# Kernel optimization log

Measured on AMD Instinct MI355X. Metric: run time of the kernel, lower is better.

The kernel has to match this reference:

```python
import jax, jax.numpy as jnp
import numpy as np

D_MODEL = 1024
HEAD_SIZE = 64
BLOCK_SIZE = 2048
B, T = 4, 2048


def setup_inputs() -> dict:
    key = jax.random.key(0)
    ks = jax.random.split(key, 7)
    s = 1.0 / np.sqrt(D_MODEL)
    x = jax.random.normal(ks[0], (B, T, D_MODEL), dtype=jnp.float32)
    Wq = jax.random.uniform(ks[1], (D_MODEL, HEAD_SIZE), jnp.float32, -s, s)
    bq = jax.random.uniform(ks[2], (HEAD_SIZE,), jnp.float32, -s, s)
    Wk = jax.random.uniform(ks[3], (D_MODEL, HEAD_SIZE), jnp.float32, -s, s)
    bk = jax.random.uniform(ks[4], (HEAD_SIZE,), jnp.float32, -s, s)
    Wv = jax.random.uniform(ks[5], (D_MODEL, HEAD_SIZE), jnp.float32, -s, s)
    return {"x": x, "Wq": Wq, "bq": bq, "Wk": Wk, "bk": bk, "Wv": Wv, "mask": 1}


def reference(x, Wq, bq, Wk, bk, Wv, mask):
    # x: [B, T, C]; single attention head, dropout is identity (eval/p=0)
    Tlen = x.shape[1]
    q = x @ Wq + bq              # [B, T, hs]
    k = x @ Wk + bk              # [B, T, hs]
    v = x @ Wv                   # [B, T, hs] (no bias)
    hs = k.shape[-1]
    # Faithful to source: weights = QK^T / hs**(-0.5)  ==  QK^T * sqrt(hs)
    w = jnp.einsum('btd,bsd->bts', q, k) * jnp.sqrt(jnp.asarray(hs, x.dtype))
    if mask:
        causal = jnp.tril(jnp.ones((Tlen, Tlen), dtype=bool))
        w = jnp.where(causal, w, jnp.asarray(-jnp.inf, w.dtype))
    w = jax.nn.softmax(w, axis=-1)
    out = jnp.einsum('bts,bsd->btd', w, v)  # [B, T, hs]
    return out
```

## Files before the change

### kernel.cpp

```cpp
#include <hip/hip_runtime.h>
#include <hip/hip_bf16.h>

#define D_MODEL 1024
#define HS 64
#define T_LEN 2048
#define JCH 256
#define NCH 8

typedef __attribute__((ext_vector_type(8))) short bf16x8;
typedef __attribute__((ext_vector_type(4))) float f32x4;

__device__ inline void split8(const float* v, int4& hi, int4& lo) {
    union { unsigned short u[8]; int4 v4; } uh, ul;
    #pragma unroll
    for (int i = 0; i < 8; ++i) {
        const unsigned int b = __float_as_uint(v[i]);
        const unsigned short h = (unsigned short)(b >> 16);
        const float r = v[i] - __uint_as_float((unsigned int)h << 16);
        uh.u[i] = h;
        ul.u[i] = (unsigned short)(__float_as_uint(r) >> 16);
    }
    hi = uh.v4; lo = ul.v4;
}

__device__ inline unsigned short f2bf_rne(float f) {
    const unsigned int b = __float_as_uint(f);
    return (unsigned short)((b + 0x7FFFu + ((b >> 16) & 1u)) >> 16);
}
__device__ inline float bf2f(unsigned short h) {
    return __uint_as_float((unsigned int)h << 16);
}

__device__ inline void async_copy16(const short* g, short* l) {
    __builtin_amdgcn_global_load_lds(
        (const __attribute__((address_space(1))) void*)g,
        (__attribute__((address_space(3))) void*)l, 16, 0, 0);
}

__global__ __launch_bounds__(256) void prep_kernel(
    const float* __restrict__ Wq, const float* __restrict__ Wk,
    const float* __restrict__ Wv,
    short* __restrict__ wh, short* __restrict__ wl)
{
    __shared__ float tile[64][69];
    const int tid = threadIdx.x;
    const int wb  = blockIdx.x;
    const int kb  = wb & 15;
    const int m   = wb >> 4;
    const float* W = (m == 0) ? Wq : (m == 1) ? Wk : Wv;
    #pragma unroll
    for (int it = 0; it < 4; ++it) {
        const int idx = tid + 256 * it;
        const int kr = idx >> 4, c4 = idx & 15;
        *(float4*)&tile[kr][4 * c4] =
            *(const float4*)(W + (size_t)(kb * 64 + kr) * HS + 4 * c4);
    }
    __syncthreads();
    #pragma unroll
    for (int i = 0; i < 2; ++i) {
        const int s    = tid + 256 * i;
        const int ntl  = s >> 7;
        const int kcl  = (s >> 6) & 1;
        const int lane = s & 63;
        const int n    = ntl * 16 + (lane & 15);
        const int krel = kcl * 32 + (lane >> 4) * 8;
        float v[8];
        #pragma unroll
        for (int e = 0; e < 8; ++e) v[e] = tile[krel + e][n];
        int4 hi, lo;
        split8(v, hi, lo);
        const size_t off =
            ((size_t)((m * 4 + ntl) * 32 + kb * 2 + kcl) * 64 + lane) * 8;
        *(int4*)(wh + off) = hi;
        *(int4*)(wl + off) = lo;
    }
}

__device__ inline void stage_B(const short* __restrict__ wh,
                               const short* __restrict__ wl,
                               short* Bdst, int ch, int wave, int lane) {
    #pragma unroll
    for (int ii = 0; ii < 12; ++ii) {
        const int g   = wave * 12 + ii;
        const int nt  = g >> 2;
        const int kcl = (g >> 1) & 1;
        const int p   = g & 1;
        const short* src = (p ? wl : wh)
                         + ((size_t)(nt * 32 + ch * 2 + kcl)) * 512;
        async_copy16(src + lane * 8, Bdst + g * 512);
    }
}

__global__ __launch_bounds__(256) void qkv_kernel(
    const float* __restrict__ x,
    const short* __restrict__ wh, const short* __restrict__ wl,
    const float* __restrict__ bq, const float* __restrict__ bk,
    short* __restrict__ qfh, short* __restrict__ qfl,
    short* __restrict__ kfh, short* __restrict__ kfl, short* __restrict__ vf)
{
    __shared__ __align__(16) short A_lds[2][8 * 512];
    __shared__ __align__(16) short B_lds[2][48 * 512];

    const int tid   = threadIdx.x;
    const int r0    = blockIdx.x * 32;
    const int wave  = tid >> 6;
    const int lane  = tid & 63;
    const int mt_l  = tid >> 7;
    const int kcl_l = (tid >> 6) & 1;
    const int nt0   = wave * 3;

    const float* xrow = x + (size_t)(r0 + mt_l * 16 + (lane & 15)) * D_MODEL
                          + kcl_l * 32 + (lane >> 4) * 8;

    f32x4 acc[2][3];
    #pragma unroll
    for (int mt = 0; mt < 2; ++mt)
        #pragma unroll
        for (int j = 0; j < 3; ++j) acc[mt][j] = (f32x4)(0.f);

    {
        stage_B(wh, wl, &B_lds[0][0], 0, wave, lane);
        float v[8];
        *(float4*)&v[0] = *(const float4*)(xrow);
        *(float4*)&v[4] = *(const float4*)(xrow + 4);
        int4 hi, lo;
        split8(v, hi, lo);
        *(int4*)&A_lds[0][(mt_l * 4 + kcl_l * 2 + 0) * 512 + lane * 8] = hi;
        *(int4*)&A_lds[0][(mt_l * 4 + kcl_l * 2 + 1) * 512 + lane * 8] = lo;
    }
    __syncthreads();

    int cur = 0;
    for (int t = 0; t < 16; ++t) {
        float v[8];
        const bool pf = (t < 15);
        if (pf) {
            *(float4*)&v[0] = *(const float4*)(xrow + (t + 1) * 64);
            *(float4*)&v[4] = *(const float4*)(xrow + (t + 1) * 64 + 4);
            stage_B(wh, wl, &B_lds[cur ^ 1][0], t + 1, wave, lane);
        }
        #pragma unroll
        for (int kcl = 0; kcl < 2; ++kcl) {
            const bf16x8 a0h = *(const bf16x8*)&A_lds[cur][(0 + kcl * 2 + 0) * 512 + lane * 8];
            const bf16x8 a0l = *(const bf16x8*)&A_lds[cur][(0 + kcl * 2 + 1) * 512 + lane * 8];
            const bf16x8 a1h = *(const bf16x8*)&A_lds[cur][(4 + kcl * 2 + 0) * 512 + lane * 8];
            const bf16x8 a1l = *(const bf16x8*)&A_lds[cur][(4 + kcl * 2 + 1) * 512 + lane * 8];
            #pragma unroll
            for (int j = 0; j < 3; ++j) {
                const int gb = (nt0 + j) * 4 + kcl * 2;
                const bf16x8 bh = *(const bf16x8*)&B_lds[cur][(gb + 0) * 512 + lane * 8];
                const bf16x8 bl = *(const bf16x8*)&B_lds[cur][(gb + 1) * 512 + lane * 8];
                acc[0][j] = __builtin_amdgcn_mfma_f32_16x16x32_bf16(a0h, bh, acc[0][j], 0, 0, 0);
                acc[0][j] = __builtin_amdgcn_mfma_f32_16x16x32_bf16(a0h, bl, acc[0][j], 0, 0, 0);
                acc[0][j] = __builtin_amdgcn_mfma_f32_16x16x32_bf16(a0l, bh, acc[0][j], 0, 0, 0);
                acc[1][j] = __builtin_amdgcn_mfma_f32_16x16x32_bf16(a1h, bh, acc[1][j], 0, 0, 0);
                acc[1][j] = __builtin_amdgcn_mfma_f32_16x16x32_bf16(a1h, bl, acc[1][j], 0, 0, 0);
                acc[1][j] = __builtin_amdgcn_mfma_f32_16x16x32_bf16(a1l, bh, acc[1][j], 0, 0, 0);
            }
        }
        if (pf) {
            int4 hi, lo;
            split8(v, hi, lo);
            *(int4*)&A_lds[cur ^ 1][(mt_l * 4 + kcl_l * 2 + 0) * 512 + lane * 8] = hi;
            *(int4*)&A_lds[cur ^ 1][(mt_l * 4 + kcl_l * 2 + 1) * 512 + lane * 8] = lo;
        }
        __syncthreads();
        cur ^= 1;
    }

    const int quad = lane >> 4;
    const int l15  = lane & 15;
    #pragma unroll
    for (int mt = 0; mt < 2; ++mt) {
        const int rowb = r0 + mt * 16 + quad * 4;
        #pragma unroll
        for (int j = 0; j < 3; ++j) {
            const f32x4 a = acc[mt][j];
            const int c = (nt0 + j) * 16 + l15;
            if (c < 128) {
                const int cc    = (c < 64) ? c : (c - 64);
                const float bias = (c < 64) ? bq[cc] : bk[cc];
                short* dsth = (c < 64) ? qfh : kfh;
                short* dstl = (c < 64) ? qfl : kfl;
                const int tile16 = rowb >> 4;
                const int kc2   = cc >> 5;
                const int quadd = (cc & 31) >> 3;
                const int e     = cc & 7;
                #pragma unroll
                for (int r = 0; r < 4; ++r) {
                    const float val = a[r] + bias;
                    const unsigned int b = __float_as_uint(val);
                    const unsigned short h = (unsigned short)(b >> 16);
                    const float res = val - __uint_as_float((unsigned int)h << 16);
                    const unsigned short l16 = (unsigned short)(__float_as_uint(res) >> 16);
                    const int laned = ((rowb + r) & 15) | (quadd << 4);
                    const size_t off = ((size_t)((tile16 * 2 + kc2) * 64 + laned)) * 8 + e;
                    dsth[off] = (short)h;
                    dstl[off] = (short)l16;
                }
            } else {
                const int cv    = c - 128;
                const int vb    = rowb >> 6;
                const int jc2   = (rowb & 63) >> 5;
                const int quadd = (rowb & 31) >> 3;
                const int gg    = jc2 * 4 + (cv >> 4);
                const int laned = (cv & 15) | (quadd << 4);
                const size_t base = ((size_t)((vb * 8 + gg) * 64 + laned)) * 8 + (rowb & 7);
                short4 pk;
                pk.x = (short)f2bf_rne(a[0]);
                pk.y = (short)f2bf_rne(a[1]);
                pk.z = (short)f2bf_rne(a[2]);
                pk.w = (short)f2bf_rne(a[3]);
                *(short4*)(vf + base) = pk;
            }
        }
    }
}

__global__ __launch_bounds__(256) void attn_kernel(
    const short* __restrict__ qfh, const short* __restrict__ qfl,
    const short* __restrict__ kfh, const short* __restrict__ kfl,
    const short* __restrict__ vf, const int* __restrict__ maskp,
    float* __restrict__ part_O, float* __restrict__ part_ml, int BT)
{
    __shared__ __align__(16) short Kh[4096], Kl[4096];
    __shared__ __align__(16) short Vt[4096];
    __shared__ __align__(16) short Pl[4][16 * 72];

    const int tile  = blockIdx.x;
    const int chunk = blockIdx.y;
    const int r0 = tile * 64;
    const int tb = r0 / T_LEN;
    const int t0 = r0 - tb * T_LEN;
    const int mask = (*maskp != 0);
    const int n_max = mask ? (t0 + 64) : T_LEN;
    const int j0 = chunk * JCH;
    if (j0 >= n_max) return;
    const int hi_j = min(j0 + JCH, n_max);
    const int njt = (hi_j - j0 + 63) >> 6;

    const int tid  = threadIdx.x;
    const int w    = tid >> 6;
    const int lane = tid & 63;
    const int quad = lane >> 4;
    const int l15  = lane & 15;
    const int rw0  = t0 + 16 * w;
    const int rowa = r0 + 16 * w + quad * 4;

    bf16x8 qh[2], ql[2];
    {
        const size_t qt = (size_t)(r0 >> 4) + w;
        #pragma unroll
        for (int kc = 0; kc < 2; ++kc) {
            qh[kc] = *(const bf16x8*)&qfh[((qt * 2 + kc) * 64 + lane) * 8];
            ql[kc] = *(const bf16x8*)&qfl[((qt * 2 + kc) * 64 + lane) * 8];
        }
    }

    f32x4 oacc[4];
    #pragma unroll
    for (int nt = 0; nt < 4; ++nt) oacc[nt] = (f32x4)(0.f);
    float m_r[4] = {-INFINITY, -INFINITY, -INFINITY, -INFINITY};
    float l_r[4] = {0.f, 0.f, 0.f, 0.f};

    for (int jt = 0; jt < njt; ++jt) {
        const int jbase = j0 + jt * 64;
        __syncthreads();
        {
            const size_t kt0 = (size_t)(tb * 128) + (jbase >> 4);
            const size_t vb  = (size_t)(tb * 32) + (jbase >> 6);
            #pragma unroll
            for (int ii = 0; ii < 6; ++ii) {
                const int g = w * 6 + ii;
                if (g < 8) {
                    const short* src = kfh + ((kt0 + (g >> 1)) * 2 + (g & 1)) * 512;
                    async_copy16(src + lane * 8, &Kh[g * 512]);
                } else if (g < 16) {
                    const int gg = g - 8;
                    const short* src = kfl + ((kt0 + (gg >> 1)) * 2 + (gg & 1)) * 512;
                    async_copy16(src + lane * 8, &Kl[gg * 512]);
                } else {
                    const int gg = g - 16;
                    const short* src = vf + (vb * 8 + gg) * 512;
                    async_copy16(src + lane * 8, &Vt[gg * 512]);
                }
            }
        }
        __syncthreads();

        const bool active = (!mask) || (jbase <= rw0 + 15);
        if (active) {
            f32x4 sacc[4];
            #pragma unroll
            for (int jsub = 0; jsub < 4; ++jsub) {
                f32x4 s = (f32x4)(0.f);
                #pragma unroll
                for (int kc = 0; kc < 2; ++kc) {
                    const bf16x8 kh = *(const bf16x8*)&Kh[((jsub * 2 + kc) * 64 + lane) * 8];
                    const bf16x8 kl = *(const bf16x8*)&Kl[((jsub * 2 + kc) * 64 + lane) * 8];
                    s = __builtin_amdgcn_mfma_f32_16x16x32_bf16(qh[kc], kh, s, 0, 0, 0);
                    s = __builtin_amdgcn_mfma_f32_16x16x32_bf16(qh[kc], kl, s, 0, 0, 0);
                    s = __builtin_amdgcn_mfma_f32_16x16x32_bf16(ql[kc], kh, s, 0, 0, 0);
                }
                sacc[jsub] = s;
            }
            float sval[4][4], rmax[4];
            #pragma unroll
            for (int r = 0; r < 4; ++r) rmax[r] = -INFINITY;
            #pragma unroll
            for (int jsub = 0; jsub < 4; ++jsub) {
                const int jg = jbase + jsub * 16 + l15;
                #pragma unroll
                for (int r = 0; r < 4; ++r) {
                    const int tg = rw0 + quad * 4 + r;
                    const float vv = (mask && (jg > tg)) ? -INFINITY : 8.0f * sacc[jsub][r];
                    sval[jsub][r] = vv;
                    rmax[r] = fmaxf(rmax[r], vv);
                }
            }
            #pragma unroll
            for (int d = 1; d < 16; d <<= 1)
                #pragma unroll
                for (int r = 0; r < 4; ++r)
                    rmax[r] = fmaxf(rmax[r], __shfl_xor(rmax[r], d));
            float alpha[4], msafe[4];
            #pragma unroll
            for (int r = 0; r < 4; ++r) {
                const float mn = fmaxf(m_r[r], rmax[r]);
                msafe[r] = (mn == -INFINITY) ? 0.f : mn;
                alpha[r] = __expf(m_r[r] - msafe[r]);
                m_r[r] = mn;
            }
            short* Pw = &Pl[w][0];
            float rsum[4] = {0.f, 0.f, 0.f, 0.f};
            #pragma unroll
            for (int jsub = 0; jsub < 4; ++jsub) {
                #pragma unroll
                for (int r = 0; r < 4; ++r) {
                    const float e = __expf(sval[jsub][r] - msafe[r]);
                    const unsigned short eb = f2bf_rne(e);
                    Pw[(quad * 4 + r) * 72 + jsub * 16 + l15] = (short)eb;
                    rsum[r] += bf2f(eb);
                }
            }
            #pragma unroll
            for (int d = 1; d < 16; d <<= 1)
                #pragma unroll
                for (int r = 0; r < 4; ++r)
                    rsum[r] += __shfl_xor(rsum[r], d);
            #pragma unroll
            for (int r = 0; r < 4; ++r)
                l_r[r] = l_r[r] * alpha[r] + rsum[r];
            #pragma unroll
            for (int nt = 0; nt < 4; ++nt)
                #pragma unroll
                for (int r = 0; r < 4; ++r)
                    oacc[nt][r] *= alpha[r];
            bf16x8 pf[2];
            #pragma unroll
            for (int jc = 0; jc < 2; ++jc)
                pf[jc] = *(const bf16x8*)&Pw[l15 * 72 + jc * 32 + quad * 8];
            #pragma unroll
            for (int nt = 0; nt < 4; ++nt) {
                #pragma unroll
                for (int jc = 0; jc < 2; ++jc) {
                    const bf16x8 vfr = *(const bf16x8*)&Vt[((jc * 4 + nt) * 64 + lane) * 8];
                    oacc[nt] = __builtin_amdgcn_mfma_f32_16x16x32_bf16(pf[jc], vfr, oacc[nt], 0, 0, 0);
                }
            }
        }
    }

    #pragma unroll
    for (int nt = 0; nt < 4; ++nt)
        #pragma unroll
        for (int r = 0; r < 4; ++r)
            part_O[((size_t)(rowa + r) * NCH + chunk) * HS + nt * 16 + l15] = oacc[nt][r];
    if (l15 == 0) {
        #pragma unroll
        for (int r = 0; r < 4; ++r) {
            float2 ml;
            ml.x = m_r[r];
            ml.y = l_r[r];
            *(float2*)(part_ml + ((size_t)(rowa + r) * NCH + chunk) * 2) = ml;
        }
    }
}

__global__ __launch_bounds__(256) void combine_kernel(
    const float* __restrict__ part_O, const float* __restrict__ part_ml,
    const int* __restrict__ maskp, float* __restrict__ out)
{
    const int f = blockIdx.x * 256 + threadIdx.x;
    const int row = f >> 4;
    const int d4 = (f & 15) * 4;
    const int t = row & (T_LEN - 1);
    const int mask = (*maskp != 0);
    const int n = mask ? (t + 1) : T_LEN;
    const int nc = (n + JCH - 1) / JCH;

    const float2* mlp = (const float2*)(part_ml + (size_t)row * NCH * 2);
    float M = -INFINITY;
    for (int c = 0; c < nc; ++c) M = fmaxf(M, mlp[c].x);
    float L = 0.f;
    float Ox = 0.f, Oy = 0.f, Oz = 0.f, Ow = 0.f;
    for (int c = 0; c < nc; ++c) {
        const float2 ml = mlp[c];
        const float w = __expf(ml.x - M);
        L += ml.y * w;
        const float4 p = *(const float4*)(part_O + ((size_t)row * NCH + c) * HS + d4);
        Ox = fmaf(p.x, w, Ox);
        Oy = fmaf(p.y, w, Oy);
        Oz = fmaf(p.z, w, Oz);
        Ow = fmaf(p.w, w, Ow);
    }
    float4 res;
    res.x = Ox / L;
    res.y = Oy / L;
    res.z = Oz / L;
    res.w = Ow / L;
    *(float4*)(out + (size_t)row * HS + d4) = res;
}

extern "C" void kernel_launch(void* const* d_in, const int* in_sizes, int n_in,
                              void* d_out, int out_size, void* d_ws, size_t ws_size,
                              hipStream_t stream) {
    const float* x  = (const float*)d_in[0];
    const float* Wq = (const float*)d_in[1];
    const float* bq = (const float*)d_in[2];
    const float* Wk = (const float*)d_in[3];
    const float* bk = (const float*)d_in[4];
    const float* Wv = (const float*)d_in[5];
    const int* maskp = (const int*)d_in[6];

    const int BT = in_sizes[0] / D_MODEL;

    float* pO  = (float*)d_ws;
    float* pml = pO + (size_t)BT * NCH * HS;
    short* wh  = (short*)(pml + (size_t)BT * NCH * 2);
    short* wl  = wh + (size_t)192 * D_MODEL;
    short* qfh = wl + (size_t)192 * D_MODEL;
    short* qfl = qfh + (size_t)BT * HS;
    short* kfh = qfl + (size_t)BT * HS;
    short* kfl = kfh + (size_t)BT * HS;
    short* vf  = kfl + (size_t)BT * HS;

    prep_kernel<<<48, 256, 0, stream>>>(Wq, Wk, Wv, wh, wl);
    qkv_kernel<<<BT / 32, 256, 0, stream>>>(x, wh, wl, bq, bk,
                                            qfh, qfl, kfh, kfl, vf);
    dim3 agrid(BT / 64, NCH);
    attn_kernel<<<agrid, 256, 0, stream>>>(qfh, qfl, kfh, kfl, vf, maskp,
                                           pO, pml, BT);
    combine_kernel<<<(BT * 16) / 256, 256, 0, stream>>>(pO, pml, maskp, (float*)d_out);
}
```

Before: 138.8 us.

## Drop LDS staging in QKV projection; load fragments directly from global

The QKV projection kernel no longer stages x and the split bf16 weights through double-buffered LDS with async copies and barriers. Each wave now loads its own x fragments and weight fragments straight from global memory into registers and splits x into hi/lo bf16 in registers. The block grows to 512 threads so each wave owns one 16-row m-tile and three n-tiles. This removes the LDS traffic and per-iteration __syncthreads, at the cost of redundant global and L2 loads of the weights across waves and no explicit prefetch.

Result: slower. 142.9 us (+2.9%).

```diff
diff --git a/kernel.cpp b/kernel.cpp
--- a/kernel.cpp
+++ b/kernel.cpp
@@ -21,6 +21,19 @@
         ul.u[i] = (unsigned short)(__float_as_uint(r) >> 16);
     }
     hi = uh.v4; lo = ul.v4;
+}
+
+__device__ inline void split8b(const float* v, bf16x8& hi, bf16x8& lo) {
+    union { unsigned short u[8]; bf16x8 v8; } uh, ul;
+    #pragma unroll
+    for (int i = 0; i < 8; ++i) {
+        const unsigned int b = __float_as_uint(v[i]);
+        const unsigned short h = (unsigned short)(b >> 16);
+        const float r = v[i] - __uint_as_float((unsigned int)h << 16);
+        uh.u[i] = h;
+        ul.u[i] = (unsigned short)(__float_as_uint(r) >> 16);
+    }
+    hi = uh.v8; lo = ul.v8;
 }
 
 __device__ inline unsigned short f2bf_rne(float f) {
@@ -76,143 +89,107 @@
     }
 }
 
-__device__ inline void stage_B(const short* __restrict__ wh,
-                               const short* __restrict__ wl,
-                               short* Bdst, int ch, int wave, int lane) {
-    #pragma unroll
-    for (int ii = 0; ii < 12; ++ii) {
-        const int g   = wave * 12 + ii;
-        const int nt  = g >> 2;
-        const int kcl = (g >> 1) & 1;
-        const int p   = g & 1;
-        const short* src = (p ? wl : wh)
-                         + ((size_t)(nt * 32 + ch * 2 + kcl)) * 512;
-        async_copy16(src + lane * 8, Bdst + g * 512);
-    }
-}
-
-__global__ __launch_bounds__(256) void qkv_kernel(
+__global__ __launch_bounds__(512, 2) void qkv_kernel(
     const float* __restrict__ x,
     const short* __restrict__ wh, const short* __restrict__ wl,
     const float* __restrict__ bq, const float* __restrict__ bk,
     short* __restrict__ qfh, short* __restrict__ qfl,
     short* __restrict__ kfh, short* __restrict__ kfl, short* __restrict__ vf)
 {
-    __shared__ __align__(16) short A_lds[2][8 * 512];
-    __shared__ __align__(16) short B_lds[2][48 * 512];
-
-    const int tid   = threadIdx.x;
-    const int r0    = blockIdx.x * 32;
-    const int wave  = tid >> 6;
-    const int lane  = tid & 63;
-    const int mt_l  = tid >> 7;
-    const int kcl_l = (tid >> 6) & 1;
-    const int nt0   = wave * 3;
-
-    const float* xrow = x + (size_t)(r0 + mt_l * 16 + (lane & 15)) * D_MODEL
-                          + kcl_l * 32 + (lane >> 4) * 8;
-
-    f32x4 acc[2][3];
-    #pragma unroll
-    for (int mt = 0; mt < 2; ++mt)
-        #pragma unroll
-        for (int j = 0; j < 3; ++j) acc[mt][j] = (f32x4)(0.f);
-
-    {
-        stage_B(wh, wl, &B_lds[0][0], 0, wave, lane);
-        float v[8];
-        *(float4*)&v[0] = *(const float4*)(xrow);
-        *(float4*)&v[4] = *(const float4*)(xrow + 4);
-        int4 hi, lo;
-        split8(v, hi, lo);
-        *(int4*)&A_lds[0][(mt_l * 4 + kcl_l * 2 + 0) * 512 + lane * 8] = hi;
-        *(int4*)&A_lds[0][(mt_l * 4 + kcl_l * 2 + 1) * 512 + lane * 8] = lo;
-    }
-    __syncthreads();
-
-    int cur = 0;
+    const int tid  = threadIdx.x;
+    const int wv   = tid >> 6;
+    const int lane = tid & 63;
+    const int mt   = wv & 1;
+    const int nt0  = (wv >> 1) * 3;
+    const int r0   = blockIdx.x * 32;
+
+    const float* xrow = x + (size_t)(r0 + mt * 16 + (lane & 15)) * D_MODEL
+                          + (lane >> 4) * 8;
+
+    f32x4 acc[3];
+    #pragma unroll
+    for (int j = 0; j < 3; ++j) acc[j] = (f32x4)(0.f);
+
+    #pragma unroll
     for (int t = 0; t < 16; ++t) {
-        float v[8];
-        const bool pf = (t < 15);
-        if (pf) {
-            *(float4*)&v[0] = *(const float4*)(xrow + (t + 1) * 64);
-            *(float4*)&v[4] = *(const float4*)(xrow + (t + 1) * 64 + 4);
-            stage_B(wh, wl, &B_lds[cur ^ 1][0], t + 1, wave, lane);
-        }
-        #pragma unroll
-        for (int kcl = 0; kcl < 2; ++kcl) {
-            const bf16x8 a0h = *(const bf16x8*)&A_lds[cur][(0 + kcl * 2 + 0) * 512 + lane * 8];
-            const bf16x8 a0l = *(const bf16x8*)&A_lds[cur][(0 + kcl * 2 + 1) * 512 + lane * 8];
-            const bf16x8 a1h = *(const bf16x8*)&A_lds[cur][(4 + kcl * 2 + 0) * 512 + lane * 8];
-            const bf16x8 a1l = *(const bf16x8*)&A_lds[cur][(4 + kcl * 2 + 1) * 512 + lane * 8];
+        const float* xc = xrow + t * 64;
+        float v0[8], v1[8];
+        *(float4*)&v0[0] = *(const float4*)(xc);
+        *(float4*)&v0[4] = *(const float4*)(xc + 4);
+        *(float4*)&v1[0] = *(const float4*)(xc + 32);
+        *(float4*)&v1[4] = *(const float4*)(xc + 36);
+
+        bf16x8 bh[2][3], bl[2][3];
+        #pragma unroll
+        for (int kcl = 0; kcl < 2; ++kcl)
             #pragma unroll
             for (int j = 0; j < 3; ++j) {
-                const int gb = (nt0 + j) * 4 + kcl * 2;
-                const bf16x8 bh = *(const bf16x8*)&B_lds[cur][(gb + 0) * 512 + lane * 8];
-                const bf16x8 bl = *(const bf16x8*)&B_lds[cur][(gb + 1) * 512 + lane * 8];
-                acc[0][j] = __builtin_amdgcn_mfma_f32_16x16x32_bf16(a0h, bh, acc[0][j], 0, 0, 0);
-                acc[0][j] = __builtin_amdgcn_mfma_f32_16x16x32_bf16(a0h, bl, acc[0][j], 0, 0, 0);
-                acc[0][j] = __builtin_amdgcn_mfma_f32_16x16x32_bf16(a0l, bh, acc[0][j], 0, 0, 0);
-                acc[1][j] = __builtin_amdgcn_mfma_f32_16x16x32_bf16(a1h, bh, acc[1][j], 0, 0, 0);
-                acc[1][j] = __builtin_amdgcn_mfma_f32_16x16x32_bf16(a1h, bl, acc[1][j], 0, 0, 0);
-                acc[1][j] = __builtin_amdgcn_mfma_f32_16x16x32_bf16(a1l, bh, acc[1][j], 0, 0, 0);
-            }
-        }
-        if (pf) {
-            int4 hi, lo;
-            split8(v, hi, lo);
-            *(int4*)&A_lds[cur ^ 1][(mt_l * 4 + kcl_l * 2 + 0) * 512 + lane * 8] = hi;
-            *(int4*)&A_lds[cur ^ 1][(mt_l * 4 + kcl_l * 2 + 1) * 512 + lane * 8] = lo;
-        }
-        __syncthreads();
-        cur ^= 1;
+                const size_t off =
+                    ((size_t)((nt0 + j) * 32 + t * 2 + kcl)) * 512 + lane * 8;
+                bh[kcl][j] = *(const bf16x8*)&wh[off];
+                bl[kcl][j] = *(const bf16x8*)&wl[off];
+            }
+
+        bf16x8 a0h, a0l, a1h, a1l;
+        split8b(v0, a0h, a0l);
+        split8b(v1, a1h, a1l);
+
+        #pragma unroll
+        for (int j = 0; j < 3; ++j) {
+            acc[j] = __builtin_amdgcn_mfma_f32_16x16x32_bf16(a0h, bh[0][j], acc[j], 0, 0, 0);
+            acc[j] = __builtin_amdgcn_mfma_f32_16x16x32_bf16(a0h, bl[0][j], acc[j], 0, 0, 0);
+            acc[j] = __builtin_amdgcn_mfma_f32_16x16x32_bf16(a0l, bh[0][j], acc[j], 0, 0, 0);
+        }
+        #pragma unroll
+        for (int j = 0; j < 3; ++j) {
+            acc[j] = __builtin_amdgcn_mfma_f32_16x16x32_bf16(a1h, bh[1][j], acc[j], 0, 0, 0);
+            acc[j] = __builtin_amdgcn_mfma_f32_16x16x32_bf16(a1h, bl[1][j], acc[j], 0, 0, 0);
+            acc[j] = __builtin_amdgcn_mfma_f32_16x16x32_bf16(a1l, bh[1][j], acc[j], 0, 0, 0);
+        }
     }
 
     const int quad = lane >> 4;
     const int l15  = lane & 15;
-    #pragma unroll
-    for (int mt = 0; mt < 2; ++mt) {
-        const int rowb = r0 + mt * 16 + quad * 4;
-        #pragma unroll
-        for (int j = 0; j < 3; ++j) {
-            const f32x4 a = acc[mt][j];
-            const int c = (nt0 + j) * 16 + l15;
-            if (c < 128) {
-                const int cc    = (c < 64) ? c : (c - 64);
-                const float bias = (c < 64) ? bq[cc] : bk[cc];
-                short* dsth = (c < 64) ? qfh : kfh;
-                short* dstl = (c < 64) ? qfl : kfl;
-                const int tile16 = rowb >> 4;
-                const int kc2   = cc >> 5;
-                const int quadd = (cc & 31) >> 3;
-                const int e     = cc & 7;
-                #pragma unroll
-                for (int r = 0; r < 4; ++r) {
-                    const float val = a[r] + bias;
-                    const unsigned int b = __float_as_uint(val);
-                    const unsigned short h = (unsigned short)(b >> 16);
-                    const float res = val - __uint_as_float((unsigned int)h << 16);
-                    const unsigned short l16 = (unsigned short)(__float_as_uint(res) >> 16);
-                    const int laned = ((rowb + r) & 15) | (quadd << 4);
-                    const size_t off = ((size_t)((tile16 * 2 + kc2) * 64 + laned)) * 8 + e;
-                    dsth[off] = (short)h;
-                    dstl[off] = (short)l16;
-                }
-            } else {
-                const int cv    = c - 128;
-                const int vb    = rowb >> 6;
-                const int jc2   = (rowb & 63) >> 5;
-                const int quadd = (rowb & 31) >> 3;
-                const int gg    = jc2 * 4 + (cv >> 4);
-                const int laned = (cv & 15) | (quadd << 4);
-                const size_t base = ((size_t)((vb * 8 + gg) * 64 + laned)) * 8 + (rowb & 7);
-                short4 pk;
-                pk.x = (short)f2bf_rne(a[0]);
-                pk.y = (short)f2bf_rne(a[1]);
-                pk.z = (short)f2bf_rne(a[2]);
-                pk.w = (short)f2bf_rne(a[3]);
-                *(short4*)(vf + base) = pk;
-            }
+    const int rowb = r0 + mt * 16 + quad * 4;
+    #pragma unroll
+    for (int j = 0; j < 3; ++j) {
+        const f32x4 a = acc[j];
+        const int c = (nt0 + j) * 16 + l15;
+        if (c < 128) {
+            const int cc    = (c < 64) ? c : (c - 64);
+            const float bias = (c < 64) ? bq[cc] : bk[cc];
+            short* dsth = (c < 64) ? qfh : kfh;
+            short* dstl = (c < 64) ? qfl : kfl;
+            const int tile16 = rowb >> 4;
+            const int kc2   = cc >> 5;
+            const int quadd = (cc & 31) >> 3;
+            const int e     = cc & 7;
+            #pragma unroll
+            for (int r = 0; r < 4; ++r) {
+                const float val = a[r] + bias;
+                const unsigned int b = __float_as_uint(val);
+                const unsigned short h = (unsigned short)(b >> 16);
+                const float res = val - __uint_as_float((unsigned int)h << 16);
+                const unsigned short l16 = (unsigned short)(__float_as_uint(res) >> 16);
+                const int laned = ((rowb + r) & 15) | (quadd << 4);
+                const size_t off = ((size_t)((tile16 * 2 + kc2) * 64 + laned)) * 8 + e;
+                dsth[off] = (short)h;
+                dstl[off] = (short)l16;
+            }
+        } else {
+            const int cv    = c - 128;
+            const int vb    = rowb >> 6;
+            const int jc2   = (rowb & 63) >> 5;
+            const int quadd = (rowb & 31) >> 3;
+            const int gg    = jc2 * 4 + (cv >> 4);
+            const int laned = (cv & 15) | (quadd << 4);
+            const size_t base = ((size_t)((vb * 8 + gg) * 64 + laned)) * 8 + (rowb & 7);
+            short4 pk;
+            pk.x = (short)f2bf_rne(a[0]);
+            pk.y = (short)f2bf_rne(a[1]);
+            pk.z = (short)f2bf_rne(a[2]);
+            pk.w = (short)f2bf_rne(a[3]);
+            *(short4*)(vf + base) = pk;
         }
     }
 }
@@ -446,7 +423,7 @@
     short* vf  = kfl + (size_t)BT * HS;
 
     prep_kernel<<<48, 256, 0, stream>>>(Wq, Wk, Wv, wh, wl);
-    qkv_kernel<<<BT / 32, 256, 0, stream>>>(x, wh, wl, bq, bk,
+    qkv_kernel<<<BT / 32, 512, 0, stream>>>(x, wh, wl, bq, bk,
                                             qfh, qfl, kfh, kfl, vf);
     dim3 agrid(BT / 64, NCH);
     attn_kernel<<<agrid, 256, 0, stream>>>(qfh, qfl, kfh, kfl, vf, maskp,
```
